# Performance work log

Measured on AMD Instinct MI355X. Metric: run time of the kernel, lower is better.

Reference implementation:

```python
import jax, jax.numpy as jnp
import numpy as np

B, T = 32, 1024
INPUT_SIZE = 512
HIDDEN = 512       # projection size
CELL = 4096        # LSTM cell size
LAYERS = 2
CLIP_C = 3.0       # memory_cell_clip_value
CLIP_H = 3.0       # state_projection_clip_value


def setup_inputs() -> dict:
    key = jax.random.key(0)
    k0, k1, k2, k3 = jax.random.split(key, 4)
    inputs = jax.random.normal(k0, (B, T, INPUT_SIZE), jnp.float32)
    mask = jnp.ones((B, T), jnp.int32)
    # Per-layer params of LstmCellWithProjection:
    #   input_linearity:  [4*cell, hidden] no bias
    #   state_linearity:  [4*cell, hidden] with bias
    #   state_projection: [hidden, cell]   no bias
    W_i = jax.random.normal(k1, (LAYERS, 4 * CELL, HIDDEN), jnp.float32) * 0.02
    W_s = jax.random.normal(k2, (LAYERS, 4 * CELL, HIDDEN), jnp.float32) * 0.02
    b_s = jnp.zeros((LAYERS, 4 * CELL), jnp.float32)
    W_p = jax.random.normal(k3, (LAYERS, HIDDEN, CELL), jnp.float32) * 0.02
    return {"inputs": inputs, "mask": mask, "W_i": W_i, "W_s": W_s,
            "b_s": b_s, "W_p": W_p}


def _lstm_layer(x, lengths, Wi, Ws, bs, Wp):
    """LstmCellWithProjection over time. x: [B,T,H] -> outs [B,T,H], hT [B,H], cT [B,C]."""
    Bb, Tt, _ = x.shape
    h0 = jnp.zeros((Bb, HIDDEN), x.dtype)
    c0 = jnp.zeros((Bb, CELL), x.dtype)
    xs = jnp.swapaxes(x, 0, 1)          # [T,B,H]
    ts = jnp.arange(Tt)

    def step(carry, inp):
        h_prev, c_prev = carry
        xt, t = inp
        gates = xt @ Wi.T + h_prev @ Ws.T + bs          # [B, 4*C]
        ig, fg, mg, og = jnp.split(gates, 4, axis=-1)   # order: input, forget, memory, output
        i = jax.nn.sigmoid(ig)
        f = jax.nn.sigmoid(fg)
        g = jnp.tanh(mg)
        o = jax.nn.sigmoid(og)
        c = jnp.clip(i * g + f * c_prev, -CLIP_C, CLIP_C)
        h = jnp.clip((o * jnp.tanh(c)) @ Wp.T, -CLIP_H, CLIP_H)
        valid = (t < lengths)[:, None]                  # [B,1]
        h_new = jnp.where(valid, h, h_prev)
        c_new = jnp.where(valid, c, c_prev)
        out = jnp.where(valid, h, 0.0)
        return (h_new, c_new), out

    (hT, cT), outs = jax.lax.scan(step, (h0, c0), (xs, ts))
    return jnp.swapaxes(outs, 0, 1), hT, cT


def reference(inputs, mask, W_i, W_s, b_s, W_p):
    lengths = jnp.sum(mask, axis=1)     # [B]
    seq = inputs                        # hidden_size == input_size -> no input projection
    outs, hs, cs = [], [], []
    for l in range(LAYERS):
        cache = seq
        seq, hT, cT = _lstm_layer(seq, lengths, W_i[l], W_s[l], b_s[l], W_p[l])
        if l != 0:
            seq = seq + cache           # ELMo residual skip connection
        outs.append(seq)
        hs.append(hT)
        cs.append(cT)
    returned = outs[-1]                 # [B,T,H] (last layer, restoration = identity)
    final_h = jnp.stack(hs)             # [L,B,H]
    final_c = jnp.stack(cs)             # [L,B,C]
    return returned, final_h, final_c
```

## Files before the change

kernel.cpp:

```cpp
#include <hip/hip_runtime.h>


#define TT 1024
#define HH 512
#define CC 4096

typedef __bf16 bf16_t;
typedef __attribute__((ext_vector_type(8))) __bf16 bf16x8;
typedef __attribute__((ext_vector_type(4))) __bf16 bf16x4;
typedef __attribute__((ext_vector_type(2))) __bf16 bf16x2;
typedef __attribute__((ext_vector_type(4))) float f32x4;
typedef unsigned long long ull_t;

#define OUT_FH 16777216u
#define OUT_FC 16809984u

__device__ __forceinline__ float fsigm(float x) { return 1.0f / (1.0f + __expf(-x)); }
__device__ __forceinline__ float ftanh(float x) {
  x = fminf(fmaxf(x, -15.f), 15.f);
  float e = __expf(2.f * x);
  return (e - 1.f) / (e + 1.f);
}

__device__ __forceinline__ void st_ull(void* p, ull_t v) {
  __hip_atomic_store((ull_t*)p, v, __ATOMIC_RELAXED, __HIP_MEMORY_SCOPE_AGENT);
}
__device__ __forceinline__ ull_t ld_ull(const void* p) {
  return __hip_atomic_load((const ull_t*)p, __ATOMIC_RELAXED, __HIP_MEMORY_SCOPE_AGENT);
}
__device__ __forceinline__ void st_f32(float* p, float v) {
  __hip_atomic_store(p, v, __ATOMIC_RELAXED, __HIP_MEMORY_SCOPE_AGENT);
}
__device__ __forceinline__ float ld_f32(const float* p) {
  return __hip_atomic_load(p, __ATOMIC_RELAXED, __HIP_MEMORY_SCOPE_AGENT);
}
__device__ __forceinline__ void st_u16(void* p, unsigned short v) {
  __hip_atomic_store((unsigned short*)p, v, __ATOMIC_RELAXED, __HIP_MEMORY_SCOPE_AGENT);
}
__device__ __forceinline__ unsigned short ld_u16(const void* p) {
  return __hip_atomic_load((const unsigned short*)p, __ATOMIC_RELAXED,
                           __HIP_MEMORY_SCOPE_AGENT);
}

__device__ __forceinline__ void gridbar(unsigned* base, int wgi, unsigned bark) {
  __syncthreads();
  if (threadIdx.x == 0)
    __hip_atomic_fetch_add(base + (wgi & 7) * 64, 1u, __ATOMIC_RELAXED,
                           __HIP_MEMORY_SCOPE_AGENT);
  if (threadIdx.x < 8) {
    const unsigned tgt = 16u * bark;
    while (__hip_atomic_load(base + threadIdx.x * 64, __ATOMIC_RELAXED,
                             __HIP_MEMORY_SCOPE_AGENT) < tgt)
      __builtin_amdgcn_s_sleep(1);
  }
  __syncthreads();
}

__global__ void prep(const int* __restrict__ mask, int* __restrict__ len,
                     unsigned* __restrict__ cnt) {
  const int b = blockIdx.x, tid = threadIdx.x;
  if (b == 0)
    for (int i = tid; i < 1024; i += 256)
      __hip_atomic_store(cnt + i, 0u, __ATOMIC_RELAXED, __HIP_MEMORY_SCOPE_AGENT);
  int s = 0;
  for (int i = tid; i < TT; i += 256) s += mask[b * TT + i];
  __shared__ int r[256];
  r[tid] = s; __syncthreads();
  for (int st = 128; st > 0; st >>= 1) {
    if (tid < st) r[tid] += r[tid + st];
    __syncthreads();
  }
  if (tid == 0) len[b] = r[0];
}

__global__ __launch_bounds__(512, 2) void elmo_lstm(
    const float* __restrict__ xin,
    const float* __restrict__ Wi_g, const float* __restrict__ Ws_g,
    const float* __restrict__ bs_g, const float* __restrict__ Wp_g,
    float* __restrict__ out,
    unsigned* __restrict__ cnt, const int* __restrict__ len_g,
    bf16_t* __restrict__ P, bf16_t* __restrict__ hbuf) {
  const int g    = blockIdx.x;
  const int L    = g >> 7;
  const int wgi  = g & 127;
  const int cb   = wgi * 32;
  const int tid  = threadIdx.x;
  const int wv   = tid >> 6;
  const int gate = wv >> 1;
  const int mt   = wv & 1;
  const int lane = tid & 63;
  const int lm   = lane & 15;
  const int lq   = lane >> 4;
  const int pb   = wgi * 4;

  __shared__ __align__(16) char uA[33024];
  __shared__ float  gbuf[4][32][33];
  __shared__ float  cbuf[32][33];
  __shared__ bf16_t abuf[32][48];
  __shared__ int    lenl[32];

  bf16_t (*xh)[1032]   = (bf16_t(*)[1032])uA;
  float  (*rbuf)[4][4] = (float(*)[4][4])uA;

  if (tid < 32) lenl[tid] = len_g[tid];

  unsigned* myc = cnt + L * 512;
  unsigned* c1  = cnt;

  const float* WiL = Wi_g + (size_t)L * CC * 4 * HH;
  const float* WsL = Ws_g + (size_t)L * CC * 4 * HH;
  const float* bsL = bs_g + (size_t)L * CC * 4;
  const float* WpL = Wp_g + (size_t)L * HH * CC;

  bf16x8 wfrag[32];
  {
    const int row = gate * CC + cb + mt * 16 + lm;
#pragma unroll
    for (int ks = 0; ks < 32; ++ks) {
      const int k = ks * 32 + lq * 8;
      const float* src = (k < HH) ? (WiL + (size_t)row * HH + k)
                                  : (WsL + (size_t)row * HH + (k - HH));
      float4 a = ((const float4*)src)[0];
      float4 b = ((const float4*)src)[1];
      bf16x8 f;
      f[0] = (bf16_t)a.x; f[1] = (bf16_t)a.y; f[2] = (bf16_t)a.z; f[3] = (bf16_t)a.w;
      f[4] = (bf16_t)b.x; f[5] = (bf16_t)b.y; f[6] = (bf16_t)b.z; f[7] = (bf16_t)b.w;
      wfrag[ks] = f;
    }
  }
  float biasv[4];
#pragma unroll
  for (int r = 0; r < 4; ++r)
    biasv[r] = bsL[gate * CC + cb + mt * 16 + lq * 4 + r];

  bf16x8 pfrag[4];
#pragma unroll
  for (int pt = 0; pt < 4; ++pt) {
    const float* src = WpL + (size_t)(wv * 64 + pt * 16 + lm) * CC + cb + lq * 8;
    float4 a = ((const float4*)src)[0];
    float4 b = ((const float4*)src)[1];
    bf16x8 f;
    f[0] = (bf16_t)a.x; f[1] = (bf16_t)a.y; f[2] = (bf16_t)a.z; f[3] = (bf16_t)a.w;
    f[4] = (bf16_t)b.x; f[5] = (bf16_t)b.y; f[6] = (bf16_t)b.z; f[7] = (bf16_t)b.w;
    pfrag[pt] = f;
  }

  for (int i = tid; i < 32 * 33; i += 512) (&cbuf[0][0])[i] = 0.f;
  bf16_t* hb = hbuf + (size_t)L * 32 * HH;
  if (tid < 128) {
    int n = tid >> 2, p = pb + (tid & 3);
    st_u16(hb + (size_t)n * HH + p, 0);
  }
  unsigned bark = 0;
  gridbar(myc, wgi, ++bark);

  const float* xsrc = (L == 0) ? xin : out;
  bf16_t* Pl = P + (size_t)L * 128 * 32 * HH;
  float hp = 0.f;

#pragma unroll 1
  for (int t = 0; t < TT; ++t) {
    if (L == 1) {
      if (tid < 8) {
        const unsigned tgt = 16u * (2u * (unsigned)t + 3u);
        while (__hip_atomic_load(c1 + tid * 64, __ATOMIC_RELAXED,
                                 __HIP_MEMORY_SCOPE_AGENT) < tgt)
          __builtin_amdgcn_s_sleep(1);
      }
      __syncthreads();
    }

    f32x4 acc0, acc1;
#pragma unroll
    for (int nh = 0; nh < 2; ++nh) {
      {
        const int r = tid & 15, q = tid >> 4;
        const int n = nh * 16 + r;
        if (q < 16) {
          const int co = q * 32;
          const float* xs = xsrc + ((size_t)n * TT + t) * HH + co;
          if (L == 0) {
#pragma unroll
            for (int i = 0; i < 8; ++i) {
              float4 v = ((const float4*)xs)[i];
              bf16x4 pv = { (bf16_t)v.x, (bf16_t)v.y, (bf16_t)v.z, (bf16_t)v.w };
              *(bf16x4*)&xh[r][co + i * 4] = pv;
            }
          } else {
            const ull_t* xu = (const ull_t*)xs;
#pragma unroll
            for (int i = 0; i < 16; ++i) {
              float2 v = __builtin_bit_cast(float2, ld_ull(xu + i));
              bf16x2 pv = { (bf16_t)v.x, (bf16_t)v.y };
              *(bf16x2*)&xh[r][co + i * 2] = pv;
            }
          }
        } else {
          const int co = (q - 16) * 32;
          const ull_t* hs = (const ull_t*)(hb + (size_t)n * HH + co);
#pragma unroll
          for (int i = 0; i < 8; ++i)
            *(ull_t*)&xh[r][HH + co + i * 4] = ld_ull(hs + i);
        }
      }
      __syncthreads();
      f32x4 a = { biasv[0], biasv[1], biasv[2], biasv[3] };
#pragma unroll
      for (int ks = 0; ks < 32; ++ks) {
        bf16x8 bfr = *(const bf16x8*)&xh[lm][ks * 32 + lq * 8];
        a = __builtin_amdgcn_mfma_f32_16x16x32_bf16(wfrag[ks], bfr, a, 0, 0, 0);
      }
      if (nh == 0) acc0 = a; else acc1 = a;
      __syncthreads();
    }

    {
      const int crow = mt * 16;
#pragma unroll
      for (int r = 0; r < 4; ++r) {
        gbuf[gate][crow + lq * 4 + r][lm]      = acc0[r];
        gbuf[gate][crow + lq * 4 + r][16 + lm] = acc1[r];
      }
    }
    __syncthreads();

#pragma unroll
    for (int e = 0; e < 2; ++e) {
      const int pp = tid * 2 + e;
      const int cell = pp >> 5, n = pp & 31;
      float ig = gbuf[0][cell][n], fg = gbuf[1][cell][n];
      float mg = gbuf[2][cell][n], og = gbuf[3][cell][n];
      float iv = fsigm(ig), fv = fsigm(fg), gv = ftanh(mg), ov = fsigm(og);
      float cp = cbuf[cell][n];
      float c  = fminf(fmaxf(iv * gv + fv * cp, -3.f), 3.f);
      const bool valid = t < lenl[n];
      float cn = valid ? c : cp;
      cbuf[cell][n] = cn;
      abuf[n][cell] = (bf16_t)(ov * ftanh(c));
      if (t == lenl[n] - 1)
        st_f32(out + OUT_FC + ((size_t)(L * 32 + n)) * CC + cb + cell, cn);
    }
    __syncthreads();

    {
      bf16x8 b0 = *(const bf16x8*)&abuf[lm][lq * 8];
      bf16x8 b1 = *(const bf16x8*)&abuf[16 + lm][lq * 8];
#pragma unroll
      for (int pt = 0; pt < 4; ++pt) {
        f32x4 p0 = { 0.f, 0.f, 0.f, 0.f };
        f32x4 p1 = { 0.f, 0.f, 0.f, 0.f };
        p0 = __builtin_amdgcn_mfma_f32_16x16x32_bf16(pfrag[pt], b0, p0, 0, 0, 0);
        p1 = __builtin_amdgcn_mfma_f32_16x16x32_bf16(pfrag[pt], b1, p1, 0, 0, 0);
        const int prow = wv * 64 + pt * 16 + lq * 4;
        bf16x4 s0 = { (bf16_t)p0[0], (bf16_t)p0[1], (bf16_t)p0[2], (bf16_t)p0[3] };
        bf16x4 s1 = { (bf16_t)p1[0], (bf16_t)p1[1], (bf16_t)p1[2], (bf16_t)p1[3] };
        st_ull(&Pl[((size_t)(wgi * 32 + lm)      * HH) + prow],
               __builtin_bit_cast(ull_t, s0));
        st_ull(&Pl[((size_t)(wgi * 32 + 16 + lm) * HH) + prow],
               __builtin_bit_cast(ull_t, s1));
      }
    }
    gridbar(myc, wgi, ++bark);

    {
      const int n = tid >> 4, pi = (tid >> 2) & 3, s = tid & 3;
      float sum = 0.f;
#pragma unroll 8
      for (int w2 = s * 32; w2 < s * 32 + 32; ++w2) {
        union { unsigned short u; bf16_t b; } cv;
        cv.u = ld_u16(&Pl[((size_t)(w2 * 32 + n)) * HH + pb + pi]);
        sum += (float)cv.b;
      }
      rbuf[n][pi][s] = sum;
    }
    __syncthreads();
    if (tid < 128) {
      const int n = tid >> 2, pi = tid & 3, p = pb + pi;
      float h = rbuf[n][pi][0] + rbuf[n][pi][1] + rbuf[n][pi][2] + rbuf[n][pi][3];
      h = fminf(fmaxf(h, -3.f), 3.f);
      const bool valid = t < lenl[n];
      float hn = valid ? h : hp;
      union { bf16_t b; unsigned short u; } hu; hu.b = (bf16_t)hn;
      st_u16(hb + (size_t)n * HH + p, hu.u);
      float outv = valid ? h : 0.f;
      size_t oi = ((size_t)n * TT + t) * HH + p;
      if (L == 0) {
        st_f32(out + oi, outv);
      } else {
        float prev = ld_f32(out + oi);
        out[oi] = prev + outv;
      }
      if (t == lenl[n] - 1)
        st_f32(out + OUT_FH + ((size_t)(L * 32 + n)) * HH + p, hn);
      hp = hn;
    }
    gridbar(myc, wgi, ++bark);
  }
}

extern "C" void kernel_launch(void* const* d_in, const int* in_sizes, int n_in,
                              void* d_out, int out_size, void* d_ws, size_t ws_size,
                              hipStream_t stream) {
  const float* xin = (const float*)d_in[0];
  const int*   mask = (const int*)d_in[1];
  const float* Wi  = (const float*)d_in[2];
  const float* Ws  = (const float*)d_in[3];
  const float* bs  = (const float*)d_in[4];
  const float* Wp  = (const float*)d_in[5];
  float* out = (float*)d_out;
  char* ws = (char*)d_ws;

  unsigned* cnt = (unsigned*)ws;
  int* len      = (int*)(ws + 4096);
  bf16_t* P    = (bf16_t*)(ws + 8192);
  bf16_t* hbuf = (bf16_t*)(ws + 8192 + (size_t)2 * 128 * 32 * 512 * 2);

  prep<<<32, 256, 0, stream>>>(mask, len, cnt);
  elmo_lstm<<<256, 512, 0, stream>>>(xin, Wi, Ws, bs, Wp, out, cnt, len, P, hbuf);
}
```

Before: 32.46 ms.

## Prefetch next-step inputs during grid barrier and vectorize projection reduction

Splits the end-of-step grid barrier into arrive and wait phases and loads the next timestep's x (or layer-0 output) into registers in between, so global load latency overlaps the barrier spin. The hidden-state and residual loads are issued up front at the start of each step. The cross-workgroup projection reduction now has 128 threads each issue 64-bit loads of four bf16 values and keep them in flight as a batch, replacing 512 threads doing scalar 16-bit loads. This raises register pressure through the xp and v arrays, and layer 1 now waits on layer 0's counter inside the barrier window.

```diff
diff --git a/kernel.cpp b/kernel.cpp
--- a/kernel.cpp
+++ b/kernel.cpp
@@ -8,7 +8,6 @@
 typedef __bf16 bf16_t;
 typedef __attribute__((ext_vector_type(8))) __bf16 bf16x8;
 typedef __attribute__((ext_vector_type(4))) __bf16 bf16x4;
-typedef __attribute__((ext_vector_type(2))) __bf16 bf16x2;
 typedef __attribute__((ext_vector_type(4))) float f32x4;
 typedef unsigned long long ull_t;
 
@@ -36,10 +35,6 @@
 }
 __device__ __forceinline__ void st_u16(void* p, unsigned short v) {
   __hip_atomic_store((unsigned short*)p, v, __ATOMIC_RELAXED, __HIP_MEMORY_SCOPE_AGENT);
-}
-__device__ __forceinline__ unsigned short ld_u16(const void* p) {
-  return __hip_atomic_load((const unsigned short*)p, __ATOMIC_RELAXED,
-                           __HIP_MEMORY_SCOPE_AGENT);
 }
 
 __device__ __forceinline__ void gridbar(unsigned* base, int wgi, unsigned bark) {
@@ -92,6 +87,8 @@
   const int lm   = lane & 15;
   const int lq   = lane >> 4;
   const int pb   = wgi * 4;
+  const int sr   = tid & 15;
+  const int sq   = tid >> 4;
 
   __shared__ __align__(16) char uA[33024];
   __shared__ float  gbuf[4][32][33];
@@ -154,53 +151,93 @@
   unsigned bark = 0;
   gridbar(myc, wgi, ++bark);
 
-  const float* xsrc = (L == 0) ? xin : out;
   bf16_t* Pl = P + (size_t)L * 128 * 32 * HH;
   float hp = 0.f;
+  bf16x4 xp[16];
+
+  auto prefetch_x = [&](int tn) {
+    if (sq < 16) {
+      const int co = sq * 32;
+      if (L == 0) {
+        const float* x0 = xin + ((size_t)sr * TT + tn) * HH + co;
+        const float* x1 = xin + ((size_t)(16 + sr) * TT + tn) * HH + co;
+#pragma unroll
+        for (int i = 0; i < 8; ++i) {
+          float4 v = ((const float4*)x0)[i];
+          bf16x4 pv = { (bf16_t)v.x, (bf16_t)v.y, (bf16_t)v.z, (bf16_t)v.w };
+          xp[i] = pv;
+        }
+#pragma unroll
+        for (int i = 0; i < 8; ++i) {
+          float4 v = ((const float4*)x1)[i];
+          bf16x4 pv = { (bf16_t)v.x, (bf16_t)v.y, (bf16_t)v.z, (bf16_t)v.w };
+          xp[8 + i] = pv;
+        }
+      } else {
+        const ull_t* x0 = (const ull_t*)(out + ((size_t)sr * TT + tn) * HH + co);
+        const ull_t* x1 = (const ull_t*)(out + ((size_t)(16 + sr) * TT + tn) * HH + co);
+#pragma unroll
+        for (int i = 0; i < 8; ++i) {
+          float2 a = __builtin_bit_cast(float2, ld_ull(x0 + 2 * i));
+          float2 b = __builtin_bit_cast(float2, ld_ull(x0 + 2 * i + 1));
+          bf16x4 pv = { (bf16_t)a.x, (bf16_t)a.y, (bf16_t)b.x, (bf16_t)b.y };
+          xp[i] = pv;
+        }
+#pragma unroll
+        for (int i = 0; i < 8; ++i) {
+          float2 a = __builtin_bit_cast(float2, ld_ull(x1 + 2 * i));
+          float2 b = __builtin_bit_cast(float2, ld_ull(x1 + 2 * i + 1));
+          bf16x4 pv = { (bf16_t)a.x, (bf16_t)a.y, (bf16_t)b.x, (bf16_t)b.y };
+          xp[8 + i] = pv;
+        }
+      }
+    }
+  };
+
+  if (L == 1) {
+    if (tid < 8) {
+      while (__hip_atomic_load(c1 + tid * 64, __ATOMIC_RELAXED,
+                               __HIP_MEMORY_SCOPE_AGENT) < 16u * 3u)
+        __builtin_amdgcn_s_sleep(1);
+    }
+    __syncthreads();
+  }
+  prefetch_x(0);
 
 #pragma unroll 1
   for (int t = 0; t < TT; ++t) {
-    if (L == 1) {
-      if (tid < 8) {
-        const unsigned tgt = 16u * (2u * (unsigned)t + 3u);
-        while (__hip_atomic_load(c1 + tid * 64, __ATOMIC_RELAXED,
-                                 __HIP_MEMORY_SCOPE_AGENT) < tgt)
-          __builtin_amdgcn_s_sleep(1);
-      }
-      __syncthreads();
-    }
+    ull_t h0v[8], h1v[8];
+    if (sq >= 16) {
+      const int co = (sq - 16) * 32;
+#pragma unroll
+      for (int i = 0; i < 8; ++i)
+        h0v[i] = ld_ull(hb + (size_t)sr * HH + co + i * 4);
+#pragma unroll
+      for (int i = 0; i < 8; ++i)
+        h1v[i] = ld_ull(hb + (size_t)(16 + sr) * HH + co + i * 4);
+    }
+    float resv = 0.f;
+    if (L == 1 && tid < 128)
+      resv = ld_f32(out + ((size_t)(tid >> 2) * TT + t) * HH + pb + (tid & 3));
 
     f32x4 acc0, acc1;
 #pragma unroll
     for (int nh = 0; nh < 2; ++nh) {
-      {
-        const int r = tid & 15, q = tid >> 4;
-        const int n = nh * 16 + r;
-        if (q < 16) {
-          const int co = q * 32;
-          const float* xs = xsrc + ((size_t)n * TT + t) * HH + co;
-          if (L == 0) {
-#pragma unroll
-            for (int i = 0; i < 8; ++i) {
-              float4 v = ((const float4*)xs)[i];
-              bf16x4 pv = { (bf16_t)v.x, (bf16_t)v.y, (bf16_t)v.z, (bf16_t)v.w };
-              *(bf16x4*)&xh[r][co + i * 4] = pv;
-            }
-          } else {
-            const ull_t* xu = (const ull_t*)xs;
-#pragma unroll
-            for (int i = 0; i < 16; ++i) {
-              float2 v = __builtin_bit_cast(float2, ld_ull(xu + i));
-              bf16x2 pv = { (bf16_t)v.x, (bf16_t)v.y };
-              *(bf16x2*)&xh[r][co + i * 2] = pv;
-            }
-          }
+      if (sq < 16) {
+        const int co = sq * 32;
+#pragma unroll
+        for (int i = 0; i < 8; ++i)
+          *(bf16x4*)&xh[sr][co + i * 4] = xp[nh * 8 + i];
+      } else {
+        const int co = (sq - 16) * 32;
+        if (nh == 0) {
+#pragma unroll
+          for (int i = 0; i < 8; ++i)
+            *(ull_t*)&xh[sr][HH + co + i * 4] = h0v[i];
         } else {
-          const int co = (q - 16) * 32;
-          const ull_t* hs = (const ull_t*)(hb + (size_t)n * HH + co);
 #pragma unroll
           for (int i = 0; i < 8; ++i)
-            *(ull_t*)&xh[r][HH + co + i * 4] = ld_ull(hs + i);
+            *(ull_t*)&xh[sr][HH + co + i * 4] = h1v[i];
         }
       }
       __syncthreads();
@@ -262,16 +299,29 @@
     }
     gridbar(myc, wgi, ++bark);
 
-    {
-      const int n = tid >> 4, pi = (tid >> 2) & 3, s = tid & 3;
-      float sum = 0.f;
-#pragma unroll 8
-      for (int w2 = s * 32; w2 < s * 32 + 32; ++w2) {
-        union { unsigned short u; bf16_t b; } cv;
-        cv.u = ld_u16(&Pl[((size_t)(w2 * 32 + n)) * HH + pb + pi]);
-        sum += (float)cv.b;
-      }
-      rbuf[n][pi][s] = sum;
+    if (tid < 128) {
+      const int n = tid >> 2, s = tid & 3;
+      const bf16_t* Pb = Pl + ((size_t)(s * 32 * 32 + n)) * HH + pb;
+      f32x4 sum = { 0.f, 0.f, 0.f, 0.f };
+      ull_t v[16];
+#pragma unroll
+      for (int j = 0; j < 16; ++j) v[j] = ld_ull(Pb + (size_t)j * 32 * HH);
+#pragma unroll
+      for (int j = 0; j < 16; ++j) {
+        bf16x4 b = __builtin_bit_cast(bf16x4, v[j]);
+        sum[0] += (float)b[0]; sum[1] += (float)b[1];
+        sum[2] += (float)b[2]; sum[3] += (float)b[3];
+      }
+#pragma unroll
+      for (int j = 0; j < 16; ++j) v[j] = ld_ull(Pb + (size_t)(16 + j) * 32 * HH);
+#pragma unroll
+      for (int j = 0; j < 16; ++j) {
+        bf16x4 b = __builtin_bit_cast(bf16x4, v[j]);
+        sum[0] += (float)b[0]; sum[1] += (float)b[1];
+        sum[2] += (float)b[2]; sum[3] += (float)b[3];
+      }
+      rbuf[n][0][s] = sum[0]; rbuf[n][1][s] = sum[1];
+      rbuf[n][2][s] = sum[2]; rbuf[n][3][s] = sum[3];
     }
     __syncthreads();
     if (tid < 128) {
@@ -284,17 +334,38 @@
       st_u16(hb + (size_t)n * HH + p, hu.u);
       float outv = valid ? h : 0.f;
       size_t oi = ((size_t)n * TT + t) * HH + p;
-      if (L == 0) {
-        st_f32(out + oi, outv);
-      } else {
-        float prev = ld_f32(out + oi);
-        out[oi] = prev + outv;
-      }
+      if (L == 0) st_f32(out + oi, outv);
+      else        out[oi] = resv + outv;
       if (t == lenl[n] - 1)
         st_f32(out + OUT_FH + ((size_t)(L * 32 + n)) * HH + p, hn);
       hp = hn;
     }
-    gridbar(myc, wgi, ++bark);
+
+    {
+      const unsigned bk = ++bark;
+      __syncthreads();
+      if (tid == 0)
+        __hip_atomic_fetch_add(myc + (wgi & 7) * 64, 1u, __ATOMIC_RELAXED,
+                               __HIP_MEMORY_SCOPE_AGENT);
+      const bool pf = (t + 1 < TT);
+      if (pf && L == 1) {
+        if (tid < 8) {
+          const unsigned tgt = 16u * (2u * (unsigned)(t + 1) + 3u);
+          while (__hip_atomic_load(c1 + tid * 64, __ATOMIC_RELAXED,
+                                   __HIP_MEMORY_SCOPE_AGENT) < tgt)
+            __builtin_amdgcn_s_sleep(1);
+        }
+        __syncthreads();
+      }
+      if (pf) prefetch_x(t + 1);
+      if (tid < 8) {
+        const unsigned tgt = 16u * bk;
+        while (__hip_atomic_load(myc + tid * 64, __ATOMIC_RELAXED,
+                                 __HIP_MEMORY_SCOPE_AGENT) < tgt)
+          __builtin_amdgcn_s_sleep(1);
+      }
+      __syncthreads();
+    }
   }
 }
 
```

Measured after the change: 36.77 ms. 13.2% more time.
